# Kernel optimization log

Hardware: AMD Instinct MI355X
Metric: run time of the kernel (lower is better)

Reference implementation:

```python
import jax, jax.numpy as jnp
import numpy as np

B, T, DFEAT = 2, 2048, 1024
DIM, DEPTH, H, DH = 512, 2, 8, 64
INNER = H * DH  # 512
MLP = 512
RED1, RED2 = DIM // 16, DIM // 32  # 32, 16
EPS = 1e-5


def _ln(x, g, b):
    m = jnp.mean(x, axis=-1, keepdims=True)
    v = jnp.mean((x - m) ** 2, axis=-1, keepdims=True)
    return (x - m) * jax.lax.rsqrt(v + EPS) * g + b


def _bn_eval(x, g, b, rm, rv):
    # x: [B, C, T]; eval-mode BatchNorm1d with running stats
    return (x - rm[:, None]) * jax.lax.rsqrt(rv[:, None] + EPS) * g[:, None] + b[:, None]


def setup_inputs() -> dict:
    key = jax.random.key(0)
    ks = iter(jax.random.split(key, 64))
    rn = lambda shape, s=0.02: (jax.random.normal(next(ks), shape, dtype=jnp.float32) * s)
    inp = {}
    inp['x'] = jax.random.normal(next(ks), (B, T, DFEAT), dtype=jnp.float32)
    # Temporal embedding conv (k=3, pad=1), OIW layout
    inp['emb_w'] = rn((DIM, DFEAT, 3))
    inp['emb_b'] = jnp.zeros((DIM,), jnp.float32)
    # Transformer: stacked per-layer params [DEPTH, ...]
    inp['ln1_g'] = jnp.ones((DEPTH, DIM), jnp.float32)
    inp['ln1_b'] = jnp.zeros((DEPTH, DIM), jnp.float32)
    inp['wqkvt'] = rn((DEPTH, DIM, 4 * INNER))
    inp['wout'] = rn((DEPTH, 2 * INNER, DIM))
    inp['bout'] = jnp.zeros((DEPTH, DIM), jnp.float32)
    inp['ln2_g'] = jnp.ones((DEPTH, DIM), jnp.float32)
    inp['ln2_b'] = jnp.zeros((DEPTH, DIM), jnp.float32)
    inp['w1'] = rn((DEPTH, DIM, MLP))
    inp['b1'] = jnp.zeros((DEPTH, MLP), jnp.float32)
    inp['w2'] = rn((DEPTH, MLP, DIM))
    inp['b2'] = jnp.zeros((DEPTH, DIM), jnp.float32)
    # NormalHead (k=1 convs -> pointwise), eval-mode BN params
    inp['h1_w'] = rn((RED1, DIM)); inp['h1_b'] = jnp.zeros((RED1,), jnp.float32)
    inp['bn1_g'] = jnp.ones((RED1,), jnp.float32); inp['bn1_b'] = jnp.zeros((RED1,), jnp.float32)
    inp['bn1_m'] = jnp.zeros((RED1,), jnp.float32); inp['bn1_v'] = jnp.ones((RED1,), jnp.float32)
    inp['h2_w'] = rn((RED2, RED1)); inp['h2_b'] = jnp.zeros((RED2,), jnp.float32)
    inp['bn2_g'] = jnp.ones((RED2,), jnp.float32); inp['bn2_b'] = jnp.zeros((RED2,), jnp.float32)
    inp['bn2_m'] = jnp.zeros((RED2,), jnp.float32); inp['bn2_v'] = jnp.ones((RED2,), jnp.float32)
    inp['h3_w'] = rn((1, RED2)); inp['h3_b'] = jnp.zeros((1,), jnp.float32)
    return inp


def _attention(x, wqkvt, wout, bout, attn2):
    b, n, d = x.shape
    qkvt = x @ wqkvt  # [b, n, 4*INNER]
    q, k, v, t = jnp.split(qkvt, 4, axis=-1)
    sp = lambda z: z.reshape(b, n, H, DH).transpose(0, 2, 1, 3)  # b h n d
    q, k, v, t = sp(q), sp(k), sp(v), sp(t)
    scale = DH ** -0.5
    dots = jnp.einsum('bhid,bhjd->bhij', q, k) * scale
    attn1 = jax.nn.softmax(dots, axis=-1)
    out1 = jnp.einsum('bhij,bhjd->bhid', attn1, v)
    out2 = jnp.einsum('ij,bhjd->bhid', attn2, t)
    out = jnp.concatenate([out1, out2], axis=-1)  # b h n 2*DH
    out = out.transpose(0, 2, 1, 3).reshape(b, n, 2 * INNER)
    return out @ wout + bout


def _forward(x, emb_w, emb_b, ln1_g, ln1_b, wqkvt, wout, bout, ln2_g, ln2_b,
             w1, b1, w2, b2, h1_w, h1_b, bn1_g, bn1_b, bn1_m, bn1_v,
             h2_w, h2_b, bn2_g, bn2_b, bn2_m, bn2_v, h3_w, h3_b):
    # Temporal embedding: Conv1d(k=3,pad=1) + ReLU over time axis
    xc = x.transpose(0, 2, 1)  # [B, DFEAT, T]
    emb = jax.lax.conv_general_dilated(xc, emb_w, (1,), 'SAME',
                                       dimension_numbers=('NCH', 'OIH', 'NCH'))
    emb = jax.nn.relu(emb + emb_b[None, :, None])
    h = emb.transpose(0, 2, 1)  # [B, T, DIM]
    # fixed temporal-decay attention matrix (batch/head independent)
    idx = jnp.arange(T, dtype=jnp.float32)
    tg = jnp.abs(idx[None, :] - idx[:, None])
    a2 = jnp.exp(-tg / jnp.float32(np.e))
    attn2 = a2 / a2.sum(-1)  # torch broadcast: divide along last axis
    for l in range(DEPTH):
        h = h + _attention(_ln(h, ln1_g[l], ln1_b[l]), wqkvt[l], wout[l], bout[l], attn2)
        z = _ln(h, ln2_g[l], ln2_b[l])
        z = jax.nn.gelu(z @ w1[l] + b1[l], approximate=False) @ w2[l] + b2[l]
        h = h + z
    # NormalHead on [B, DIM, T] with k=1 convs
    y = h.transpose(0, 2, 1)
    f1 = jnp.einsum('oc,bct->bot', h1_w, y) + h1_b[None, :, None]
    f2 = jnp.einsum('oc,bct->bot', h2_w, jax.nn.relu(_bn_eval(f1, bn1_g, bn1_b, bn1_m, bn1_v))) + h2_b[None, :, None]
    f3 = jnp.einsum('oc,bct->bot', h3_w, jax.nn.relu(_bn_eval(f2, bn2_g, bn2_b, bn2_m, bn2_v))) + h3_b[None, :, None]
    scores = jax.nn.sigmoid(f3)[:, 0, :]  # [B, T]
    return scores


def reference(x, emb_w, emb_b, ln1_g, ln1_b, wqkvt, wout, bout, ln2_g, ln2_b,
              w1, b1, w2, b2, h1_w, h1_b, bn1_g, bn1_b, bn1_m, bn1_v,
              h2_w, h2_b, bn2_g, bn2_b, bn2_m, bn2_v, h3_w, h3_b):
    return _forward(x, emb_w, emb_b, ln1_g, ln1_b, wqkvt, wout, bout, ln2_g, ln2_b,
                    w1, b1, w2, b2, h1_w, h1_b, bn1_g, bn1_b, bn1_m, bn1_v,
                    h2_w, h2_b, bn2_g, bn2_b, bn2_m, bn2_v, h3_w, h3_b)
```

## Files before the change

### kernel.cpp

```cpp
#include <hip/hip_runtime.h>
#include <hip/hip_bf16.h>
#include <math.h>

#define TN 2048
#define BN 2
#define DF 1024
#define DM 512
#define NHD 8
#define DHD 64
#define INV_E 0.36787944117144233f
#define R_DECAY 0.69220062755534635f

typedef float f32x4 __attribute__((ext_vector_type(4)));
typedef __bf16 bf16x8 __attribute__((ext_vector_type(8)));
typedef unsigned short ushort8 __attribute__((ext_vector_type(8)));
typedef unsigned short ushort4v __attribute__((ext_vector_type(4)));
typedef unsigned int u32x4 __attribute__((ext_vector_type(4)));
typedef unsigned short u16;
typedef unsigned int u32;

__device__ inline u16 f2bf(float f) {
    __hip_bfloat16 b = __float2bfloat16(f);
    return __builtin_bit_cast(u16, b);
}
__device__ inline float bf2f(u16 u) {
    unsigned int x = ((unsigned int)u) << 16;
    return __builtin_bit_cast(float, x);
}
__device__ inline bf16x8 ldbf8(const u16* p) {
    return __builtin_bit_cast(bf16x8, *(const ushort8*)p);
}

struct WtrAll {
    const float* src[8];
    u16* dst[8];
    int K[8], N[8], start[8], mask[8], shift[8];
};

__global__ __launch_bounds__(256) void wtr_all_kernel(WtrAll a) {
    __shared__ u16 tile[64][67];
    int bid = blockIdx.x;
    int w = 0;
#pragma unroll
    for (int i = 1; i < 8; ++i)
        if (bid >= a.start[i]) w = i;
    const float* src = a.src[w];
    u16* dst = a.dst[w];
    int K = a.K[w], N = a.N[w];
    int t0 = bid - a.start[w];
    int bx = t0 & a.mask[w], by = t0 >> a.shift[w];
    int t = threadIdx.x;
    int tr = t >> 4, tc = (t & 15) * 4;
#pragma unroll
    for (int rr = 0; rr < 4; ++rr) {
        int kl = tr + rr * 16;
        float4 v = *(const float4*)&src[(size_t)(by * 64 + kl) * N + bx * 64 + tc];
        tile[kl][tc + 0] = f2bf(v.x);
        tile[kl][tc + 1] = f2bf(v.y);
        tile[kl][tc + 2] = f2bf(v.z);
        tile[kl][tc + 3] = f2bf(v.w);
    }
    __syncthreads();
#pragma unroll
    for (int rr = 0; rr < 4; ++rr) {
        int nl = tr + rr * 16;
        ushort4v o;
#pragma unroll
        for (int q = 0; q < 4; ++q) o[q] = tile[tc + q][nl];
        *(ushort4v*)&dst[(size_t)(bx * 64 + nl) * K + by * 64 + tc] = o;
    }
}

__global__ __launch_bounds__(256) void emb_tr_kernel(const float* __restrict__ w,
                                                     u16* __restrict__ dst) {
    int idx = blockIdx.x * 256 + threadIdx.x;
    if (idx >= DM * 3 * DF) return;
    int o = idx / (3 * DF);
    int rem = idx - o * 3 * DF;
    int tap = rem / DF, i = rem - tap * DF;
    dst[idx] = f2bf(w[(size_t)o * 3 * DF + i * 3 + tap]);
}

__global__ __launch_bounds__(256) void sinv_kernel(float* __restrict__ sinv) {
    int j = blockIdx.x * 256 + threadIdx.x;
    if (j >= TN) return;
    float r = __expf(-INV_E);
    float inv1mr = 1.f / (1.f - r);
    float a = (1.f - __expf(-(float)(j + 1) * INV_E)) * inv1mr;
    float b = (r - __expf(-(float)(TN - j) * INV_E)) * inv1mr;
    sinv[j] = 1.f / (a + b);
}

__global__ __launch_bounds__(256) void xshift_kernel(const float* __restrict__ x,
                                                     u16* __restrict__ xs) {
    int idx = blockIdx.x * 256 + threadIdx.x;
    if (idx >= BN * TN * 3 * DF / 8) return;
    int row = idx / (3 * DF / 8);
    int kc = (idx - row * (3 * DF / 8)) * 8;
    int b = row >> 11, t = row & (TN - 1);
    int tap = kc / DF, i = kc - tap * DF;
    int tt = t + tap - 1;
    ushort8 o;
    if (tt < 0 || tt >= TN) {
        for (int q = 0; q < 8; ++q) o[q] = 0;
    } else {
        const float4* p = (const float4*)&x[((size_t)b * TN + tt) * DF + i];
        float4 v0 = p[0], v1 = p[1];
        o[0] = f2bf(v0.x); o[1] = f2bf(v0.y); o[2] = f2bf(v0.z); o[3] = f2bf(v0.w);
        o[4] = f2bf(v1.x); o[5] = f2bf(v1.y); o[6] = f2bf(v1.z); o[7] = f2bf(v1.w);
    }
    *(ushort8*)&xs[(size_t)row * 3 * DF + kc] = o;
}

template <int MODE, int BM, int BNT>
__global__ __launch_bounds__(256) void gemm2(const u16* __restrict__ A,
                                             const u16* __restrict__ Bt,
                                             const float* __restrict__ bias,
                                             const float* resid, void* outp,
                                             int M, int N, int K) {
    constexpr int MR = BM / 32, NR = BNT / 32;
    constexpr int PA = BM / 64, PB = BNT / 64;
    __shared__ __align__(16) u16 As[2][BM][72];
    __shared__ __align__(16) u16 Bs[2][BNT][72];
    int tid = threadIdx.x;
    int lane = tid & 63, wid = tid >> 6;
    int m0 = blockIdx.y * BM, n0 = blockIdx.x * BNT;
    int wm = (wid >> 1) * (BM / 2), wn = (wid & 1) * (BNT / 2);
    int fr = lane & 15, kq = (lane >> 4) * 8;
    int srow = tid >> 2, scol = (tid & 3) * 16;
    f32x4 acc[MR][NR] = {};
    const u16* Ap = A + (size_t)(m0 + srow) * K + scol;
    const u16* Bp = Bt + (size_t)(n0 + srow) * K + scol;
    ushort8 ra[PA][2], rb[PB][2];
#pragma unroll
    for (int p = 0; p < PA; ++p) {
        ra[p][0] = *(const ushort8*)(Ap + (size_t)p * 64 * K);
        ra[p][1] = *(const ushort8*)(Ap + (size_t)p * 64 * K + 8);
    }
#pragma unroll
    for (int p = 0; p < PB; ++p) {
        rb[p][0] = *(const ushort8*)(Bp + (size_t)p * 64 * K);
        rb[p][1] = *(const ushort8*)(Bp + (size_t)p * 64 * K + 8);
    }
    int nt = K >> 6;
    int pb = 0;
    for (int t = 0; t < nt; ++t) {
#pragma unroll
        for (int p = 0; p < PA; ++p) {
            *(ushort8*)&As[pb][srow + p * 64][scol] = ra[p][0];
            *(ushort8*)&As[pb][srow + p * 64][scol + 8] = ra[p][1];
        }
#pragma unroll
        for (int p = 0; p < PB; ++p) {
            *(ushort8*)&Bs[pb][srow + p * 64][scol] = rb[p][0];
            *(ushort8*)&Bs[pb][srow + p * 64][scol + 8] = rb[p][1];
        }
        __syncthreads();
        if (t + 1 < nt) {
            int ko = (t + 1) << 6;
#pragma unroll
            for (int p = 0; p < PA; ++p) {
                ra[p][0] = *(const ushort8*)(Ap + (size_t)p * 64 * K + ko);
                ra[p][1] = *(const ushort8*)(Ap + (size_t)p * 64 * K + ko + 8);
            }
#pragma unroll
            for (int p = 0; p < PB; ++p) {
                rb[p][0] = *(const ushort8*)(Bp + (size_t)p * 64 * K + ko);
                rb[p][1] = *(const ushort8*)(Bp + (size_t)p * 64 * K + ko + 8);
            }
        }
#pragma unroll
        for (int kc = 0; kc < 2; ++kc) {
            bf16x8 af[MR], bf[NR];
#pragma unroll
            for (int a = 0; a < MR; ++a) af[a] = ldbf8(&As[pb][wm + a * 16 + fr][kc * 32 + kq]);
#pragma unroll
            for (int b = 0; b < NR; ++b) bf[b] = ldbf8(&Bs[pb][wn + b * 16 + fr][kc * 32 + kq]);
#pragma unroll
            for (int a = 0; a < MR; ++a)
#pragma unroll
                for (int b = 0; b < NR; ++b)
                    acc[a][b] = __builtin_amdgcn_mfma_f32_16x16x32_bf16(af[a], bf[b], acc[a][b], 0, 0, 0);
        }
        pb ^= 1;
    }
    int rq = (lane >> 4) * 4;
#pragma unroll
    for (int a = 0; a < MR; ++a)
#pragma unroll
        for (int b = 0; b < NR; ++b) {
            int col = n0 + wn + b * 16 + fr;
            float bv = (MODE & 1) ? bias[col] : 0.f;
#pragma unroll
            for (int r = 0; r < 4; ++r) {
                int row = m0 + wm + a * 16 + rq + r;
                float v = acc[a][b][r] + bv;
                if (MODE & 2) v = fmaxf(v, 0.f);
                if (MODE & 4) v = 0.5f * v * (1.f + erff(v * 0.7071067811865476f));
                if (MODE & 8) v += resid[(size_t)row * N + col];
                if (MODE & 16) ((float*)outp)[(size_t)row * N + col] = v;
                else           ((u16*)outp)[(size_t)row * N + col] = f2bf(v);
            }
        }
}

__global__ __launch_bounds__(256) void ln_kernel(const float* __restrict__ h,
                                                 const float* __restrict__ g,
                                                 const float* __restrict__ bta,
                                                 u16* __restrict__ outp) {
    int lane = threadIdx.x & 63, wid = threadIdx.x >> 6;
    int row = blockIdx.x * 4 + wid;
    const float4* xp = (const float4*)(h + (size_t)row * DM + lane * 8);
    float4 v0 = xp[0], v1 = xp[1];
    float v[8] = {v0.x, v0.y, v0.z, v0.w, v1.x, v1.y, v1.z, v1.w};
    float s = 0.f;
#pragma unroll
    for (int i = 0; i < 8; ++i) s += v[i];
    for (int sft = 1; sft < 64; sft <<= 1) s += __shfl_xor(s, sft, 64);
    float mean = s * (1.f / DM);
    float q = 0.f;
#pragma unroll
    for (int i = 0; i < 8; ++i) { float d = v[i] - mean; q += d * d; }
    for (int sft = 1; sft < 64; sft <<= 1) q += __shfl_xor(q, sft, 64);
    float rs = rsqrtf(q * (1.f / DM) + 1e-5f);
    ushort8 o;
#pragma unroll
    for (int i = 0; i < 8; ++i) {
        float y = (v[i] - mean) * rs * g[lane * 8 + i] + bta[lane * 8 + i];
        o[i] = f2bf(y);
    }
    *(ushort8*)&outp[(size_t)row * DM + lane * 8] = o;
}

__global__ __launch_bounds__(256, 4) void attn_split(const u16* __restrict__ qkvt,
                                                     u16* __restrict__ po,
                                                     float* __restrict__ pl) {
    __shared__ __align__(16) u16 Ks[2][64][72];
    __shared__ __align__(16) u16 Vs[2][64][72];
    int tid = threadIdx.x;
    int lane = tid & 63, wid = tid >> 6;
    int bid = blockIdx.x;
    int cc = bid & 3, qb = (bid >> 2) & 31, hh = (bid >> 7) & 7, b = bid >> 10;
    int fr = lane & 15, kq = (lane >> 4) * 8, rq = (lane >> 4) * 4;

    int qrow = qb * 64 + wid * 16 + fr;
    bf16x8 aq[2];
#pragma unroll
    for (int kc = 0; kc < 2; ++kc) {
        bf16x8 t = ldbf8(&qkvt[((size_t)(b * TN + qrow)) * 2048 + hh * 64 + kc * 32 + kq]);
        bf16x8 sc;
#pragma unroll
        for (int i = 0; i < 8; ++i) sc[i] = (__bf16)(0.125f * (float)t[i]);
        aq[kc] = sc;
    }

    f32x4 o[4];
#pragma unroll
    for (int cb = 0; cb < 4; ++cb) o[cb] = f32x4{0.f, 0.f, 0.f, 0.f};
    float rsum = 0.f;

    int srow = tid >> 3, scol = (tid & 7) * 8;
    int vxw = ((scol >> 3) & 7) << 3;
    int i01 = (fr + ((lane & 16) << 1)) << 2;
    int i23 = i01 + 64;
    bool hi2 = (lane & 32) != 0;

    ushort8 rk[2], rv[2];
#pragma unroll
    for (int half = 0; half < 2; ++half) {
        int jr = srow + half * 32;
        size_t rbase = ((size_t)(b * TN + cc * 512 + jr)) * 2048;
        rk[half] = *(const ushort8*)&qkvt[rbase + 512 + hh * 64 + scol];
        rv[half] = *(const ushort8*)&qkvt[rbase + 1024 + hh * 64 + scol];
    }
    int cur = 0;
#pragma unroll
    for (int half = 0; half < 2; ++half) {
        int jr = srow + half * 32;
        *(ushort8*)&Ks[0][jr][scol] = rk[half];
        int jc = jr ^ vxw;
#pragma unroll
        for (int i = 0; i < 8; ++i) Vs[0][scol + i][jc] = rv[half][i];
    }

    for (int t = 0; t < 8; ++t) {
        if (t < 7) {
            int j0 = cc * 512 + (t + 1) * 64;
#pragma unroll
            for (int half = 0; half < 2; ++half) {
                int jr = srow + half * 32;
                size_t rbase = ((size_t)(b * TN + j0 + jr)) * 2048;
                rk[half] = *(const ushort8*)&qkvt[rbase + 512 + hh * 64 + scol];
                rv[half] = *(const ushort8*)&qkvt[rbase + 1024 + hh * 64 + scol];
            }
        }
        __syncthreads();
        float p[4][4];
#pragma unroll
        for (int jb = 0; jb < 4; ++jb) {
            f32x4 sa = f32x4{0.f, 0.f, 0.f, 0.f};
#pragma unroll
            for (int kc = 0; kc < 2; ++kc) {
                bf16x8 bk = ldbf8(&Ks[cur][jb * 16 + fr][kc * 32 + kq]);
                sa = __builtin_amdgcn_mfma_f32_16x16x32_bf16(bk, aq[kc], sa, 0, 0, 0);
            }
#pragma unroll
            for (int r = 0; r < 4; ++r) {
                p[jb][r] = __expf(sa[r]);
                rsum += p[jb][r];
            }
        }
        u32 pkr[4][2];
#pragma unroll
        for (int jb = 0; jb < 4; ++jb)
#pragma unroll
            for (int rp = 0; rp < 2; ++rp)
                pkr[jb][rp] = ((u32)f2bf(p[jb][2 * rp + 1]) << 16) | (u32)f2bf(p[jb][2 * rp]);
        bf16x8 pa[2];
#pragma unroll
        for (int kc = 0; kc < 2; ++kc) {
            u32 a0 = (u32)__builtin_amdgcn_ds_bpermute(i01, (int)pkr[kc * 2][0]);
            u32 b0 = (u32)__builtin_amdgcn_ds_bpermute(i01, (int)pkr[kc * 2 + 1][0]);
            u32 a1 = (u32)__builtin_amdgcn_ds_bpermute(i01, (int)pkr[kc * 2][1]);
            u32 b1 = (u32)__builtin_amdgcn_ds_bpermute(i01, (int)pkr[kc * 2 + 1][1]);
            u32 a2 = (u32)__builtin_amdgcn_ds_bpermute(i23, (int)pkr[kc * 2][0]);
            u32 b2 = (u32)__builtin_amdgcn_ds_bpermute(i23, (int)pkr[kc * 2 + 1][0]);
            u32 a3 = (u32)__builtin_amdgcn_ds_bpermute(i23, (int)pkr[kc * 2][1]);
            u32 b3 = (u32)__builtin_amdgcn_ds_bpermute(i23, (int)pkr[kc * 2 + 1][1]);
            u32x4 w;
            w[0] = hi2 ? b0 : a0;
            w[1] = hi2 ? b1 : a1;
            w[2] = hi2 ? b2 : a2;
            w[3] = hi2 ? b3 : a3;
            pa[kc] = __builtin_bit_cast(bf16x8, w);
        }
#pragma unroll
        for (int cb = 0; cb < 4; ++cb)
#pragma unroll
            for (int kc = 0; kc < 2; ++kc) {
                int vrow = cb * 16 + fr;
                bf16x8 bv = ldbf8(&Vs[cur][vrow][(kc * 32 + kq) ^ (((vrow >> 3) & 7) << 3)]);
                o[cb] = __builtin_amdgcn_mfma_f32_16x16x32_bf16(pa[kc], bv, o[cb], 0, 0, 0);
            }
        if (t < 7) {
            int nb = cur ^ 1;
#pragma unroll
            for (int half = 0; half < 2; ++half) {
                int jr = srow + half * 32;
                *(ushort8*)&Ks[nb][jr][scol] = rk[half];
                int jc = jr ^ vxw;
#pragma unroll
                for (int i = 0; i < 8; ++i) Vs[nb][scol + i][jc] = rv[half][i];
            }
            cur = nb;
        }
    }
    rsum += __shfl_xor(rsum, 16, 64);
    rsum += __shfl_xor(rsum, 32, 64);
#pragma unroll
    for (int r = 0; r < 4; ++r) {
        int grow = (b * NHD + hh) * TN + qb * 64 + wid * 16 + rq + r;
        size_t pidx = (size_t)grow * 4 + cc;
#pragma unroll
        for (int cb = 0; cb < 4; ++cb)
            po[pidx * 64 + cb * 16 + fr] = f2bf(o[cb][r]);
    }
    if (lane < 16) {
        int grow = (b * NHD + hh) * TN + qb * 64 + wid * 16 + fr;
        pl[(size_t)grow * 4 + cc] = rsum;
    }
}

__global__ __launch_bounds__(256) void attn_combine(const u16* __restrict__ po,
                                                    const float* __restrict__ pl,
                                                    u16* __restrict__ attcat) {
    int lane = threadIdx.x & 63, wid = threadIdx.x >> 6;
    int R = blockIdx.x * 4 + wid;
    float l = 0.f, ov = 0.f;
#pragma unroll
    for (int cc = 0; cc < 4; ++cc) {
        l += pl[R * 4 + cc];
        ov += bf2f(po[((size_t)R * 4 + cc) * 64 + lane]);
    }
    int bh = R >> 11, q = R & (TN - 1);
    int b = bh >> 3, hh = bh & 7;
    attcat[((size_t)(b * TN + q)) * 1024 + hh * 128 + lane] = f2bf(ov / l);
}

#define BCH 32
__global__ __launch_bounds__(256) void band_scan_kernel(const u16* __restrict__ qkvt,
                                                        const float* __restrict__ sinv,
                                                        u16* __restrict__ attcat) {
    int tid = blockIdx.x * 256 + threadIdx.x;
    int c = tid & 511;
    int rest = tid >> 9;
    int chunk = rest & 63;
    int b = rest >> 6;
    int i0 = chunk * BCH;
    const float r = R_DECAY;
    const u16* tcol = qkvt + 1536 + c;
    float regs[BCH];
    float st = 0.f;
    for (int j = i0 - 32; j < i0; ++j) {
        if (j >= 0) st = r * st + sinv[j] * bf2f(tcol[(size_t)(b * TN + j) * 2048]);
    }
#pragma unroll
    for (int k = 0; k < BCH; ++k) {
        int j = i0 + k;
        st = r * st + sinv[j] * bf2f(tcol[(size_t)(b * TN + j) * 2048]);
        regs[k] = st;
    }
    st = 0.f;
    for (int j = i0 + BCH + 31; j >= i0 + BCH; --j) {
        if (j < TN) st = r * st + sinv[j] * bf2f(tcol[(size_t)(b * TN + j) * 2048]);
    }
#pragma unroll
    for (int k = BCH - 1; k >= 0; --k) {
        int j = i0 + k;
        regs[k] += r * st;
        st = r * st + sinv[j] * bf2f(tcol[(size_t)(b * TN + j) * 2048]);
    }
    int outcol = (c >> 6) * 128 + 64 + (c & 63);
#pragma unroll
    for (int k = 0; k < BCH; ++k)
        attcat[((size_t)(b * TN + i0 + k)) * 1024 + outcol] = f2bf(regs[k]);
}

__global__ __launch_bounds__(256) void head_kernel(
    const float* __restrict__ h, const float* __restrict__ h1w, const float* __restrict__ h1b,
    const float* __restrict__ bn1g, const float* __restrict__ bn1b,
    const float* __restrict__ bn1m, const float* __restrict__ bn1v,
    const float* __restrict__ h2w, const float* __restrict__ h2b,
    const float* __restrict__ bn2g, const float* __restrict__ bn2b,
    const float* __restrict__ bn2m, const float* __restrict__ bn2v,
    const float* __restrict__ h3w, const float* __restrict__ h3b,
    float* __restrict__ outp) {
    int lane = threadIdx.x & 63, wid = threadIdx.x >> 6;
    int idx = blockIdx.x * 4 + wid;
    const float4* xp = (const float4*)(h + (size_t)idx * DM + lane * 8);
    float4 v0 = xp[0], v1 = xp[1];
    float v[8] = {v0.x, v0.y, v0.z, v0.w, v1.x, v1.y, v1.z, v1.w};
    float a1[32];
#pragma unroll
    for (int o = 0; o < 32; ++o) {
        const float4* wp = (const float4*)(h1w + (size_t)o * DM + lane * 8);
        float4 w0 = wp[0], w1v = wp[1];
        a1[o] = w0.x * v[0] + w0.y * v[1] + w0.z * v[2] + w0.w * v[3] +
                w1v.x * v[4] + w1v.y * v[5] + w1v.z * v[6] + w1v.w * v[7];
    }
    for (int sft = 1; sft < 64; sft <<= 1) {
#pragma unroll
        for (int o = 0; o < 32; ++o) a1[o] += __shfl_xor(a1[o], sft, 64);
    }
    float r1[32];
#pragma unroll
    for (int o = 0; o < 32; ++o) {
        float f = a1[o] + h1b[o];
        f = (f - bn1m[o]) * rsqrtf(bn1v[o] + 1e-5f) * bn1g[o] + bn1b[o];
        r1[o] = fmaxf(f, 0.f);
    }
    float r2[16];
#pragma unroll
    for (int p = 0; p < 16; ++p) {
        float s = h2b[p];
#pragma unroll
        for (int o = 0; o < 32; ++o) s = fmaf(h2w[p * 32 + o], r1[o], s);
        s = (s - bn2m[p]) * rsqrtf(bn2v[p] + 1e-5f) * bn2g[p] + bn2b[p];
        r2[p] = fmaxf(s, 0.f);
    }
    float f3 = h3b[0];
#pragma unroll
    for (int p = 0; p < 16; ++p) f3 = fmaf(h3w[p], r2[p], f3);
    if (lane == 0) outp[idx] = 1.f / (1.f + __expf(-f3));
}

extern "C" void kernel_launch(void* const* d_in, const int* in_sizes, int n_in,
                              void* d_out, int out_size, void* d_ws, size_t ws_size,
                              hipStream_t stream) {
    const float* x     = (const float*)d_in[0];
    const float* emb_w = (const float*)d_in[1];
    const float* emb_b = (const float*)d_in[2];
    const float* ln1_g = (const float*)d_in[3];
    const float* ln1_b = (const float*)d_in[4];
    const float* wqkvt = (const float*)d_in[5];
    const float* wout  = (const float*)d_in[6];
    const float* bout  = (const float*)d_in[7];
    const float* ln2_g = (const float*)d_in[8];
    const float* ln2_b = (const float*)d_in[9];
    const float* w1    = (const float*)d_in[10];
    const float* b1    = (const float*)d_in[11];
    const float* w2    = (const float*)d_in[12];
    const float* b2    = (const float*)d_in[13];
    const float* h1w   = (const float*)d_in[14];
    const float* h1b   = (const float*)d_in[15];
    const float* bn1g  = (const float*)d_in[16];
    const float* bn1b  = (const float*)d_in[17];
    const float* bn1m  = (const float*)d_in[18];
    const float* bn1v  = (const float*)d_in[19];
    const float* h2w   = (const float*)d_in[20];
    const float* h2b   = (const float*)d_in[21];
    const float* bn2g  = (const float*)d_in[22];
    const float* bn2b  = (const float*)d_in[23];
    const float* bn2m  = (const float*)d_in[24];
    const float* bn2v  = (const float*)d_in[25];
    const float* h3w   = (const float*)d_in[26];
    const float* h3b   = (const float*)d_in[27];
    float* outp = (float*)d_out;

    char* ws = (char*)d_ws;
    size_t off = 0;
    auto take = [&](size_t bytes) {
        char* p = ws + off;
        off = (off + bytes + 255) & ~(size_t)255;
        return p;
    };
    const size_t MB = 1024 * 1024;
    float* h    = (float*)take((size_t)BN * TN * DM * 4);
    char* Pr    = take(18 * MB);
    u16* attcat = (u16*)take((size_t)BN * TN * 1024 * 2);
    float* sinv = (float*)take(TN * 4);
    u16* embwt  = (u16*)take((size_t)DM * 3 * DF * 2);
    u16* wqt    = (u16*)take((size_t)2 * 2048 * DM * 2);
    u16* woutt  = (u16*)take((size_t)2 * DM * 1024 * 2);
    u16* w1t    = (u16*)take((size_t)2 * DM * DM * 2);
    u16* w2t    = (u16*)take((size_t)2 * DM * DM * 2);
    u16* U      = (u16*)take((size_t)BN * TN * 3 * DF * 2);
    u16* xs = U;
    u16* qkvtb = U;
    u16* xln  = (u16*)Pr;
    u16* z1   = (u16*)(Pr + 4 * MB);
    float* pl = (float*)Pr;
    u16* po   = (u16*)(Pr + 1 * MB);
    (void)ws_size; (void)in_sizes; (void)n_in; (void)out_size;

    emb_tr_kernel<<<dim3(DM * 3 * DF / 256), dim3(256), 0, stream>>>(emb_w, embwt);
    {
        WtrAll a;
        int cur = 0;
        for (int l = 0; l < 2; ++l) {
            int e = l * 4;
            a.src[e + 0] = wqkvt + (size_t)l * 512 * 2048; a.dst[e + 0] = wqt + (size_t)l * 2048 * 512;
            a.K[e + 0] = 512;  a.N[e + 0] = 2048; a.start[e + 0] = cur; a.mask[e + 0] = 31; a.shift[e + 0] = 5; cur += 256;
            a.src[e + 1] = wout + (size_t)l * 1024 * 512;  a.dst[e + 1] = woutt + (size_t)l * 512 * 1024;
            a.K[e + 1] = 1024; a.N[e + 1] = 512;  a.start[e + 1] = cur; a.mask[e + 1] = 7;  a.shift[e + 1] = 3; cur += 128;
            a.src[e + 2] = w1 + (size_t)l * 512 * 512;     a.dst[e + 2] = w1t + (size_t)l * 512 * 512;
            a.K[e + 2] = 512;  a.N[e + 2] = 512;  a.start[e + 2] = cur; a.mask[e + 2] = 7;  a.shift[e + 2] = 3; cur += 64;
            a.src[e + 3] = w2 + (size_t)l * 512 * 512;     a.dst[e + 3] = w2t + (size_t)l * 512 * 512;
            a.K[e + 3] = 512;  a.N[e + 3] = 512;  a.start[e + 3] = cur; a.mask[e + 3] = 7;  a.shift[e + 3] = 3; cur += 64;
        }
        wtr_all_kernel<<<dim3(cur), dim3(256), 0, stream>>>(a);
    }
    sinv_kernel<<<dim3(TN / 256), dim3(256), 0, stream>>>(sinv);
    xshift_kernel<<<dim3(BN * TN * 3 * DF / 8 / 256), dim3(256), 0, stream>>>(x, xs);

    gemm2<19, 64, 64><<<dim3(DM / 64, BN * TN / 64), dim3(256), 0, stream>>>(
        xs, embwt, emb_b, nullptr, h, BN * TN, DM, 3 * DF);

    for (int l = 0; l < 2; ++l) {
        ln_kernel<<<dim3(BN * TN / 4), dim3(256), 0, stream>>>(h, ln1_g + l * DM, ln1_b + l * DM, xln);
        gemm2<0, 128, 128><<<dim3(2048 / 128, BN * TN / 128), dim3(256), 0, stream>>>(
            xln, wqt + (size_t)l * 2048 * 512, nullptr, nullptr, qkvtb, BN * TN, 2048, DM);
        attn_split<<<dim3(BN * NHD * (TN / 64) * 4), dim3(256), 0, stream>>>(qkvtb, po, pl);
        attn_combine<<<dim3(BN * NHD * TN / 4), dim3(256), 0, stream>>>(po, pl, attcat);
        band_scan_kernel<<<dim3(BN * 512 * (TN / BCH) / 256), dim3(256), 0, stream>>>(qkvtb, sinv, attcat);
        gemm2<25, 64, 64><<<dim3(DM / 64, BN * TN / 64), dim3(256), 0, stream>>>(
            attcat, woutt + (size_t)l * 512 * 1024, bout + l * DM, h, h, BN * TN, DM, 1024);
        ln_kernel<<<dim3(BN * TN / 4), dim3(256), 0, stream>>>(h, ln2_g + l * DM, ln2_b + l * DM, xln);
        gemm2<5, 64, 64><<<dim3(DM / 64, BN * TN / 64), dim3(256), 0, stream>>>(
            xln, w1t + (size_t)l * 512 * 512, b1 + l * DM, nullptr, z1, BN * TN, DM, DM);
        gemm2<25, 64, 64><<<dim3(DM / 64, BN * TN / 64), dim3(256), 0, stream>>>(
            z1, w2t + (size_t)l * 512 * 512, b2 + l * DM, h, h, BN * TN, DM, DM);
    }
    head_kernel<<<dim3(BN * TN / 4), dim3(256), 0, stream>>>(
        h, h1w, h1b, bn1g, bn1b, bn1m, bn1v, h2w, h2b, bn2g, bn2b, bn2m, bn2v, h3w, h3b, outp);
}
```

Before: 338.1 us.

## Load attention K straight from global and merge combine with band scan kernel

In the split attention kernel, the K tile is no longer staged through shared memory. Each lane now reads its MFMA operand directly from global memory, and launch bounds rise to allow 8 blocks per CU since LDS use is halved. The attention combine and band-scan kernels are merged into one launch that dispatches on block index, which removes a launch and lets the two independent workloads overlap. The trade-off is uncoalesced, strided global reads for K (one 16-byte load per row at a 4 KB stride) that depend on cache hits, plus tighter register limits from the higher occupancy target.

Measured after the change: 436.8 us. 29.2% more time.

```diff
diff --git a/kernel.cpp b/kernel.cpp
--- a/kernel.cpp
+++ b/kernel.cpp
@@ -232,10 +232,9 @@
     *(ushort8*)&outp[(size_t)row * DM + lane * 8] = o;
 }
 
-__global__ __launch_bounds__(256, 4) void attn_split(const u16* __restrict__ qkvt,
+__global__ __launch_bounds__(256, 8) void attn_split(const u16* __restrict__ qkvt,
                                                      u16* __restrict__ po,
                                                      float* __restrict__ pl) {
-    __shared__ __align__(16) u16 Ks[2][64][72];
     __shared__ __align__(16) u16 Vs[2][64][72];
     int tid = threadIdx.x;
     int lane = tid & 63, wid = tid >> 6;
@@ -265,19 +264,18 @@
     int i23 = i01 + 64;
     bool hi2 = (lane & 32) != 0;
 
-    ushort8 rk[2], rv[2];
+    const u16* kbase = qkvt + ((size_t)(b * TN + cc * 512 + fr)) * 2048 + 512 + hh * 64 + kq;
+
+    ushort8 rv[2];
 #pragma unroll
     for (int half = 0; half < 2; ++half) {
         int jr = srow + half * 32;
-        size_t rbase = ((size_t)(b * TN + cc * 512 + jr)) * 2048;
-        rk[half] = *(const ushort8*)&qkvt[rbase + 512 + hh * 64 + scol];
-        rv[half] = *(const ushort8*)&qkvt[rbase + 1024 + hh * 64 + scol];
+        rv[half] = *(const ushort8*)&qkvt[((size_t)(b * TN + cc * 512 + jr)) * 2048 + 1024 + hh * 64 + scol];
     }
     int cur = 0;
 #pragma unroll
     for (int half = 0; half < 2; ++half) {
         int jr = srow + half * 32;
-        *(ushort8*)&Ks[0][jr][scol] = rk[half];
         int jc = jr ^ vxw;
 #pragma unroll
         for (int i = 0; i < 8; ++i) Vs[0][scol + i][jc] = rv[half][i];
@@ -289,19 +287,18 @@
 #pragma unroll
             for (int half = 0; half < 2; ++half) {
                 int jr = srow + half * 32;
-                size_t rbase = ((size_t)(b * TN + j0 + jr)) * 2048;
-                rk[half] = *(const ushort8*)&qkvt[rbase + 512 + hh * 64 + scol];
-                rv[half] = *(const ushort8*)&qkvt[rbase + 1024 + hh * 64 + scol];
+                rv[half] = *(const ushort8*)&qkvt[((size_t)(b * TN + j0 + jr)) * 2048 + 1024 + hh * 64 + scol];
             }
         }
         __syncthreads();
+        const u16* kb = kbase + (size_t)t * 64 * 2048;
         float p[4][4];
 #pragma unroll
         for (int jb = 0; jb < 4; ++jb) {
             f32x4 sa = f32x4{0.f, 0.f, 0.f, 0.f};
 #pragma unroll
             for (int kc = 0; kc < 2; ++kc) {
-                bf16x8 bk = ldbf8(&Ks[cur][jb * 16 + fr][kc * 32 + kq]);
+                bf16x8 bk = ldbf8(kb + (size_t)jb * 16 * 2048 + kc * 32);
                 sa = __builtin_amdgcn_mfma_f32_16x16x32_bf16(bk, aq[kc], sa, 0, 0, 0);
             }
 #pragma unroll
@@ -347,7 +344,6 @@
 #pragma unroll
             for (int half = 0; half < 2; ++half) {
                 int jr = srow + half * 32;
-                *(ushort8*)&Ks[nb][jr][scol] = rk[half];
                 int jc = jr ^ vxw;
 #pragma unroll
                 for (int i = 0; i < 8; ++i) Vs[nb][scol + i][jc] = rv[half][i];
@@ -371,59 +367,60 @@
     }
 }
 
-__global__ __launch_bounds__(256) void attn_combine(const u16* __restrict__ po,
-                                                    const float* __restrict__ pl,
-                                                    u16* __restrict__ attcat) {
-    int lane = threadIdx.x & 63, wid = threadIdx.x >> 6;
-    int R = blockIdx.x * 4 + wid;
-    float l = 0.f, ov = 0.f;
-#pragma unroll
-    for (int cc = 0; cc < 4; ++cc) {
-        l += pl[R * 4 + cc];
-        ov += bf2f(po[((size_t)R * 4 + cc) * 64 + lane]);
-    }
-    int bh = R >> 11, q = R & (TN - 1);
-    int b = bh >> 3, hh = bh & 7;
-    attcat[((size_t)(b * TN + q)) * 1024 + hh * 128 + lane] = f2bf(ov / l);
-}
-
 #define BCH 32
-__global__ __launch_bounds__(256) void band_scan_kernel(const u16* __restrict__ qkvt,
-                                                        const float* __restrict__ sinv,
-                                                        u16* __restrict__ attcat) {
-    int tid = blockIdx.x * 256 + threadIdx.x;
-    int c = tid & 511;
-    int rest = tid >> 9;
-    int chunk = rest & 63;
-    int b = rest >> 6;
-    int i0 = chunk * BCH;
-    const float r = R_DECAY;
-    const u16* tcol = qkvt + 1536 + c;
-    float regs[BCH];
-    float st = 0.f;
-    for (int j = i0 - 32; j < i0; ++j) {
-        if (j >= 0) st = r * st + sinv[j] * bf2f(tcol[(size_t)(b * TN + j) * 2048]);
-    }
-#pragma unroll
-    for (int k = 0; k < BCH; ++k) {
-        int j = i0 + k;
-        st = r * st + sinv[j] * bf2f(tcol[(size_t)(b * TN + j) * 2048]);
-        regs[k] = st;
-    }
-    st = 0.f;
-    for (int j = i0 + BCH + 31; j >= i0 + BCH; --j) {
-        if (j < TN) st = r * st + sinv[j] * bf2f(tcol[(size_t)(b * TN + j) * 2048]);
-    }
-#pragma unroll
-    for (int k = BCH - 1; k >= 0; --k) {
-        int j = i0 + k;
-        regs[k] += r * st;
-        st = r * st + sinv[j] * bf2f(tcol[(size_t)(b * TN + j) * 2048]);
-    }
-    int outcol = (c >> 6) * 128 + 64 + (c & 63);
-#pragma unroll
-    for (int k = 0; k < BCH; ++k)
-        attcat[((size_t)(b * TN + i0 + k)) * 1024 + outcol] = f2bf(regs[k]);
+__global__ __launch_bounds__(256) void postattn_kernel(const u16* __restrict__ po,
+                                                       const float* __restrict__ pl,
+                                                       const u16* __restrict__ qkvt,
+                                                       const float* __restrict__ sinv,
+                                                       u16* __restrict__ attcat) {
+    int bid = blockIdx.x;
+    if (bid < BN * NHD * TN / 4) {
+        int lane = threadIdx.x & 63, wid = threadIdx.x >> 6;
+        int R = bid * 4 + wid;
+        float l = 0.f, ov = 0.f;
+#pragma unroll
+        for (int cc = 0; cc < 4; ++cc) {
+            l += pl[R * 4 + cc];
+            ov += bf2f(po[((size_t)R * 4 + cc) * 64 + lane]);
+        }
+        int bh = R >> 11, q = R & (TN - 1);
+        int b = bh >> 3, hh = bh & 7;
+        attcat[((size_t)(b * TN + q)) * 1024 + hh * 128 + lane] = f2bf(ov / l);
+    } else {
+        int t2 = (bid - BN * NHD * TN / 4) * 256 + threadIdx.x;
+        int c = t2 & 511;
+        int rest = t2 >> 9;
+        int chunk = rest & 63;
+        int b = rest >> 6;
+        int i0 = chunk * BCH;
+        const float r = R_DECAY;
+        const u16* tcol = qkvt + 1536 + c;
+        float regs[BCH];
+        float st = 0.f;
+        for (int j = i0 - 32; j < i0; ++j) {
+            if (j >= 0) st = r * st + sinv[j] * bf2f(tcol[(size_t)(b * TN + j) * 2048]);
+        }
+#pragma unroll
+        for (int k = 0; k < BCH; ++k) {
+            int j = i0 + k;
+            st = r * st + sinv[j] * bf2f(tcol[(size_t)(b * TN + j) * 2048]);
+            regs[k] = st;
+        }
+        st = 0.f;
+        for (int j = i0 + BCH + 31; j >= i0 + BCH; --j) {
+            if (j < TN) st = r * st + sinv[j] * bf2f(tcol[(size_t)(b * TN + j) * 2048]);
+        }
+#pragma unroll
+        for (int k = BCH - 1; k >= 0; --k) {
+            int j = i0 + k;
+            regs[k] += r * st;
+            st = r * st + sinv[j] * bf2f(tcol[(size_t)(b * TN + j) * 2048]);
+        }
+        int outcol = (c >> 6) * 128 + 64 + (c & 63);
+#pragma unroll
+        for (int k = 0; k < BCH; ++k)
+            attcat[((size_t)(b * TN + i0 + k)) * 1024 + outcol] = f2bf(regs[k]);
+    }
 }
 
 __global__ __launch_bounds__(256) void head_kernel(
@@ -561,8 +558,8 @@
         gemm2<0, 128, 128><<<dim3(2048 / 128, BN * TN / 128), dim3(256), 0, stream>>>(
             xln, wqt + (size_t)l * 2048 * 512, nullptr, nullptr, qkvtb, BN * TN, 2048, DM);
         attn_split<<<dim3(BN * NHD * (TN / 64) * 4), dim3(256), 0, stream>>>(qkvtb, po, pl);
-        attn_combine<<<dim3(BN * NHD * TN / 4), dim3(256), 0, stream>>>(po, pl, attcat);
-        band_scan_kernel<<<dim3(BN * 512 * (TN / BCH) / 256), dim3(256), 0, stream>>>(qkvtb, sinv, attcat);
+        postattn_kernel<<<dim3(BN * NHD * TN / 4 + BN * 512 * (TN / BCH) / 256), dim3(256), 0, stream>>>(
+            po, pl, qkvtb, sinv, attcat);
         gemm2<25, 64, 64><<<dim3(DM / 64, BN * TN / 64), dim3(256), 0, stream>>>(
             attcat, woutt + (size_t)l * 512 * 1024, bout + l * DM, h, h, BN * TN, DM, 1024);
         ln_kernel<<<dim3(BN * TN / 4), dim3(256), 0, stream>>>(h, ln2_g + l * DM, ln2_b + l * DM, xln);
```
